# Kernel optimization log

Hardware: AMD Instinct MI355X
Metric: run time of the kernel (lower is better)

Reference implementation:

```python
import jax, jax.numpy as jnp
import numpy as np

# Module configuration (from init_kwargs)
N, C_IN, C_OUT, L, V, P = 4, 64, 64, 1024, 25, 3
KERNEL_SIZE, STRIDE = 9, 1
EPS = 1e-5


def _toeplitz(length):
    # Faithful to: sum_i pad(eye(L - stride*i), (i*stride, 0, 0, i*stride))
    # -> ones at [r, r + i*stride] for i in range(kernel_size // stride)
    t = jnp.zeros((length, length), dtype=jnp.float32)
    for i in range(KERNEL_SIZE // STRIDE):  # small fixed loop over taps
        t = t + jnp.eye(length, k=i * STRIDE, dtype=jnp.float32)
    return t


def setup_inputs() -> dict:
    key = jax.random.key(0)
    k0, k1, k2, k3 = jax.random.split(key, 4)
    x = jax.random.normal(k0, (N, C_IN, L, V), dtype=jnp.float32)
    A = jax.random.uniform(k1, (P, V, V), dtype=jnp.float32)
    edge_importance = jnp.ones((P, V, V), dtype=jnp.float32)
    conv_w = jax.random.normal(k2, (C_OUT * P, C_IN, 1, 1), dtype=jnp.float32) * 0.05
    conv_b = jax.random.normal(k3, (C_OUT * P,), dtype=jnp.float32) * 0.05
    gamma = jnp.ones((C_OUT,), dtype=jnp.float32)
    beta = jnp.zeros((C_OUT,), dtype=jnp.float32)
    return {"x": x, "A": A, "edge_importance": edge_importance,
            "conv_w": conv_w, "conv_b": conv_b, "gamma": gamma, "beta": beta}


def reference(x, A, edge_importance, conv_w, conv_b, gamma, beta):
    n, _, l, v = x.shape
    res = x  # residual: in_channels == out_channels and stride == 1 -> identity

    # 1x1 conv: (N, C_in, L, V) -> (N, P*C_out, L, V)
    w = conv_w[:, :, 0, 0]  # (P*C_out, C_in)
    y = jnp.einsum('nclv,kc->nklv', x, w) + conv_b[None, :, None, None]

    # split into P chunks of C_out along channels, stack, permute -> (N, L, P, C_out, V)
    y = y.reshape(n, P, C_OUT, l, v).transpose(0, 3, 1, 2, 4)

    # partition-wise graph adjacency matmul with edge-importance mask
    y = jnp.einsum('nlpcv,pvw->nlpcw', y, A * edge_importance)

    # Toeplitz temporal conv: (N, P, C, V, L) @ (L, L)
    y = y.transpose(0, 2, 3, 4, 1)
    y = jnp.matmul(y, _toeplitz(l))
    y = y.sum(axis=1)            # sum over partitions -> (N, C, V, L)
    y = y.transpose(0, 1, 3, 2)  # (N, C, L, V)

    # BatchNorm2d with batch statistics (track_running_stats=False) + ReLU
    mean = y.mean(axis=(0, 2, 3), keepdims=True)
    var = y.var(axis=(0, 2, 3), keepdims=True)  # biased, as torch uses for normalization
    y = (y - mean) * jax.lax.rsqrt(var + EPS)
    y = y * gamma[None, :, None, None] + beta[None, :, None, None]
    y = jax.nn.relu(y)

    # do = Sequential(ReLU, Dropout(0.0)) applied to (y + res)
    return jax.nn.relu(y + res)
```

## Files before the change

### kernel.cpp

```cpp
#include <hip/hip_runtime.h>
#include <hip/hip_cooperative_groups.h>

namespace cg = cooperative_groups;


typedef unsigned short ushort_t;
typedef __attribute__((ext_vector_type(8))) short short8;
typedef __attribute__((ext_vector_type(4))) float f32x4;
typedef __attribute__((ext_vector_type(4))) unsigned short us4;

#define N_  4
#define CI_ 64
#define CO_ 64
#define L_  1024
#define V_  25
#define P_  3
#define KS_ 9
#define NLV 102400.0f
#define NREP 32
#define TSTR 406

__device__ __forceinline__ float b2f(ushort_t u) {
  union { float f; unsigned int i; } c; c.i = ((unsigned int)u) << 16; return c.f;
}
__device__ __forceinline__ ushort_t f2b(float f) {
  union { float f; unsigned int i; } c; c.f = f;
  unsigned int u = c.i;
  u += 0x7fffu + ((u >> 16) & 1u);
  return (ushort_t)(u >> 16);
}
__device__ __forceinline__ unsigned int cvtpk(float lo, float hi) {
  unsigned int r;
  asm("v_cvt_pk_bf16_f32 %0, %1, %2" : "=v"(r) : "v"(lo), "v"(hi));
  return r;
}
__device__ __forceinline__ float lo2f(unsigned int u) {
  union { float f; unsigned int i; } c; c.i = u << 16; return c.f;
}
__device__ __forceinline__ float hi2f(unsigned int u) {
  union { float f; unsigned int i; } c; c.i = u & 0xffff0000u; return c.f;
}

__global__ __launch_bounds__(256) void kwin(
    const float* __restrict__ x, ushort_t* __restrict__ xs,
    const float* __restrict__ A, const float* __restrict__ E,
    const float* __restrict__ cb, const float* __restrict__ W,
    ushort_t* __restrict__ a2raw, float* __restrict__ biastab,
    ushort_t* __restrict__ wb, float* __restrict__ statsbuf)
{
  const int bx = blockIdx.x;
  const int n = blockIdx.y;
  const int tid = threadIdx.x;

  if (bx == 256) {
    if (n != 0) return;
    __shared__ float colA[P_ * 32];
    if (tid < P_ * 32) {
      int p = tid >> 5, w = tid & 31;
      float s = 0.f;
      if (w < V_)
        for (int v = 0; v < V_; ++v) {
          int idx = (p * V_ + v) * V_ + w;
          s += A[idx] * E[idx];
        }
      colA[tid] = s;
    }
    for (int e = tid; e < 32 * 96; e += 256) {
      int w = e / 96, k = e - w * 96;
      int p = k >> 5, v = k & 31;
      float val = 0.f;
      if (w < V_ && v < V_) {
        int idx = (p * V_ + v) * V_ + w;
        val = A[idx] * E[idx];
      }
      a2raw[e] = f2b(val);
    }
    for (int e = tid; e < 192 * 64; e += 256) wb[e] = f2b(W[e]);
    __syncthreads();
    for (int e = tid; e < 32 * 64; e += 256) {
      int w = e >> 6, c = e & 63;
      float s = 0.f;
      for (int p = 0; p < P_; ++p) s += cb[p * 64 + c] * colA[p * 32 + w];
      biastab[e] = s;
    }
    for (int e = tid; e < NREP * 128; e += 256) statsbuf[e] = 0.f;
    return;
  }

  const int chunk = bx >> 1, half = bx & 1;
  __shared__ __align__(16) ushort_t tile[32 * TSTR];
  const int l0 = chunk * 8;
  const long xn = (long)n * CI_ * L_ * V_ + (long)(half * 32) * (L_ * V_);
  for (int m = tid; m < 3200; m += 256) {
    int ci = m / 100;
    int j4 = (m - ci * 100) * 4;
    f32x4 d;
    if (chunk == 0 && j4 < 200) {
      d = (f32x4){0.f, 0.f, 0.f, 0.f};
    } else {
      d = *(const f32x4*)(x + xn + (long)ci * (L_ * V_) + (l0 - 8) * V_ + j4);
    }
    unsigned int p0 = (unsigned int)f2b(d[0]) | ((unsigned int)f2b(d[1]) << 16);
    unsigned int p1 = (unsigned int)f2b(d[2]) | ((unsigned int)f2b(d[3]) << 16);
    *(unsigned int*)(&tile[ci * TSTR + j4])     = p0;
    *(unsigned int*)(&tile[ci * TSTR + j4 + 2]) = p1;
  }
  __syncthreads();
  const long xsbase = ((long)n * L_ + l0) * 1600 + half * 32;
  for (int cp = tid; cp < 400; cp += 256) {
    const int v = cp >> 4, ci = (cp & 15) * 2;
    const ushort_t* c0 = &tile[ci * TSTR + v];
    const ushort_t* c1 = c0 + TSTR;
    float s0 = 0.f, s1 = 0.f;
#pragma unroll
    for (int li = 0; li < 9; ++li) { s0 += b2f(c0[li * 25]); s1 += b2f(c1[li * 25]); }
    *(unsigned int*)(xs + xsbase + v * 64 + ci) =
        (unsigned int)f2b(s0) | ((unsigned int)f2b(s1) << 16);
#pragma unroll
    for (int l_ = 1; l_ < 8; ++l_) {
      s0 += b2f(c0[(l_ + 8) * 25]) - b2f(c0[(l_ - 1) * 25]);
      s1 += b2f(c1[(l_ + 8) * 25]) - b2f(c1[(l_ - 1) * 25]);
      *(unsigned int*)(xs + xsbase + l_ * 1600 + v * 64 + ci) =
          (unsigned int)f2b(s0) | ((unsigned int)f2b(s1) << 16);
    }
  }
}

template<bool COOP>
__global__ __launch_bounds__(256, 4) void kmain(
    const float*    __restrict__ x,
    ushort_t*       __restrict__ xs,
    const float*    __restrict__ A, const float* __restrict__ E,
    const float*    __restrict__ cb, const float* __restrict__ W,
    ushort_t*       __restrict__ wb,
    ushort_t*       __restrict__ a2,
    float*          __restrict__ biastab,
    ushort_t*       __restrict__ zb,
    float*          __restrict__ statsbuf,
    const float*    __restrict__ gamma,
    const float*    __restrict__ beta,
    float*          __restrict__ out)
{
  const int lb = blockIdx.x;
  const int n  = blockIdx.y;
  const int tid = threadIdx.x, lane = tid & 63, wv = tid >> 6;
  const int m16 = lane & 15, quad = lane >> 4;

  __shared__ __align__(16) ushort_t T1[13312];
  __shared__ float colA[P_ * 32];

  if constexpr (COOP) {
    ushort_t* tile = T1;
    const int chunk = lb >> 1, half = lb & 1;
    const int l0 = chunk * 8;
    const long xn = (long)n * CI_ * L_ * V_ + (long)(half * 32) * (L_ * V_);
    for (int m = tid; m < 3200; m += 256) {
      int ci = m / 100;
      int j4 = (m - ci * 100) * 4;
      f32x4 d;
      if (chunk == 0 && j4 < 200) {
        d = (f32x4){0.f, 0.f, 0.f, 0.f};
      } else {
        d = *(const f32x4*)(x + xn + (long)ci * (L_ * V_) + (l0 - 8) * V_ + j4);
      }
      *(unsigned int*)(&tile[ci * TSTR + j4])     = cvtpk(d[0], d[1]);
      *(unsigned int*)(&tile[ci * TSTR + j4 + 2]) = cvtpk(d[2], d[3]);
    }
    if (n == 1) {
      if (lb == 0) {
        for (int e = tid; e < 32 * 96; e += 256) {
          int w = e / 96, k = e - w * 96;
          int p = k >> 5, v = k & 31;
          float val = 0.f;
          if (w < V_ && v < V_) {
            int idx = (p * V_ + v) * V_ + w;
            val = A[idx] * E[idx];
          }
          a2[e] = f2b(val);
        }
      } else if (lb == 1) {
        for (int e = tid; e < 6144; e += 256) wb[e] = f2b(W[e]);
      } else if (lb == 2) {
        for (int e = tid; e < 6144; e += 256) wb[6144 + e] = f2b(W[6144 + e]);
      } else if (lb == 3) {
        for (int e = tid; e < NREP * 128; e += 256) statsbuf[e] = 0.f;
      } else if (lb == 4) {
        if (tid < P_ * 32) {
          int p = tid >> 5, w = tid & 31;
          float s = 0.f;
          if (w < V_)
            for (int v = 0; v < V_; ++v) {
              int idx = (p * V_ + v) * V_ + w;
              s += A[idx] * E[idx];
            }
          colA[tid] = s;
        }
      }
    }
    __syncthreads();
    const long xsbase = ((long)n * L_ + l0) * 1600 + half * 32;
    for (int cp = tid; cp < 400; cp += 256) {
      const int v = cp >> 4, ci = (cp & 15) * 2;
      const ushort_t* c0 = &tile[ci * TSTR + v];
      const ushort_t* c1 = c0 + TSTR;
      float s0 = 0.f, s1 = 0.f;
#pragma unroll
      for (int li = 0; li < 9; ++li) { s0 += b2f(c0[li * 25]); s1 += b2f(c1[li * 25]); }
      *(unsigned int*)(xs + xsbase + v * 64 + ci) = cvtpk(s0, s1);
#pragma unroll
      for (int l_ = 1; l_ < 8; ++l_) {
        s0 += b2f(c0[(l_ + 8) * 25]) - b2f(c0[(l_ - 1) * 25]);
        s1 += b2f(c1[(l_ + 8) * 25]) - b2f(c1[(l_ - 1) * 25]);
        *(unsigned int*)(xs + xsbase + l_ * 1600 + v * 64 + ci) = cvtpk(s0, s1);
      }
    }
    if (n == 1 && lb == 4) {
      for (int e = tid; e < 32 * 64; e += 256) {
        int w = e >> 6, c = e & 63;
        float s = 0.f;
        for (int p = 0; p < P_; ++p) s += cb[p * 64 + c] * colA[p * 32 + w];
        biastab[e] = s;
      }
    }
    cg::this_grid().sync();
  }

  short8 af[3][2];
#pragma unroll
  for (int i = 0; i < 3; ++i) {
    const ushort_t* wrow = wb + ((wv * 3 + i) * 16 + m16) * 64 + quad * 8;
    af[i][0] = *(const short8*)(wrow);
    af[i][1] = *(const short8*)(wrow + 32);
  }

  short8 bfr2[2][3];
#pragma unroll
  for (int nt = 0; nt < 2; ++nt)
#pragma unroll
    for (int ks = 0; ks < 3; ++ks)
      bfr2[nt][ks] = *(const short8*)(a2 + (nt * 16 + m16) * 96 + ks * 32 + quad * 8);

  const int cbase = wv * 16 + quad * 4;
  f32x4 biasv[2];
#pragma unroll
  for (int nt = 0; nt < 2; ++nt)
    biasv[nt] = *(const f32x4*)(biastab + (nt * 16 + m16) * 64 + cbase);

  const ushort_t* xsb = xs + ((long)n * L_ + 4 * lb) * 1600;
  float s1[4] = {0.f, 0.f, 0.f, 0.f}, s2[4] = {0.f, 0.f, 0.f, 0.f};
  unsigned int zpk[2][2][2][2];

#pragma unroll
  for (int pair = 0; pair < 2; ++pair) {
    short8 bfr[4][2];
#pragma unroll
    for (int nt = 0; nt < 4; ++nt) {
      const int v = (nt & 1) * 16 + m16;
      const int l_ = pair * 2 + (nt >> 1);
#pragma unroll
      for (int ks = 0; ks < 2; ++ks) {
        short8 t = (short8){0, 0, 0, 0, 0, 0, 0, 0};
        if (v < V_)
          t = *(const short8*)(xsb + l_ * 1600 + v * 64 + ks * 32 + quad * 8);
        bfr[nt][ks] = t;
      }
    }

    f32x4 acc1[3][4];
#pragma unroll
    for (int i = 0; i < 3; ++i)
#pragma unroll
      for (int j = 0; j < 4; ++j) acc1[i][j] = (f32x4){0.f, 0.f, 0.f, 0.f};

#pragma unroll
    for (int i = 0; i < 3; ++i)
#pragma unroll
      for (int nt = 0; nt < 4; ++nt) {
        acc1[i][nt] = __builtin_amdgcn_mfma_f32_16x16x32_bf16(af[i][0], bfr[nt][0], acc1[i][nt], 0, 0, 0);
        acc1[i][nt] = __builtin_amdgcn_mfma_f32_16x16x32_bf16(af[i][1], bfr[nt][1], acc1[i][nt], 0, 0, 0);
      }

    __syncthreads();
#pragma unroll
    for (int i = 0; i < 3; ++i) {
      const int mt = wv * 3 + i;
#pragma unroll
      for (int nt = 0; nt < 4; ++nt) {
        const int l_ = nt >> 1;
        const int col = (nt & 1) * 16 + m16;
#pragma unroll
        for (int r = 0; r < 4; ++r) {
          int k = mt * 16 + quad * 4 + r;
          T1[l_ * 6656 + (k & 63) * 104 + (k >> 6) * 32 + col] = f2b(acc1[i][nt][r]);
        }
      }
    }
    __syncthreads();

    f32x4 acc2[2][2];
#pragma unroll
    for (int l_ = 0; l_ < 2; ++l_)
#pragma unroll
      for (int nt = 0; nt < 2; ++nt) acc2[l_][nt] = (f32x4){0.f, 0.f, 0.f, 0.f};

#pragma unroll
    for (int l_ = 0; l_ < 2; ++l_)
#pragma unroll
      for (int ks = 0; ks < 3; ++ks) {
        short8 afT = *(const short8*)(&T1[l_ * 6656 + (wv * 16 + m16) * 104 + ks * 32 + quad * 8]);
        acc2[l_][0] = __builtin_amdgcn_mfma_f32_16x16x32_bf16(afT, bfr2[0][ks], acc2[l_][0], 0, 0, 0);
        acc2[l_][1] = __builtin_amdgcn_mfma_f32_16x16x32_bf16(afT, bfr2[1][ks], acc2[l_][1], 0, 0, 0);
      }

#pragma unroll
    for (int l_ = 0; l_ < 2; ++l_) {
      const int l = 4 * lb + pair * 2 + l_;
      const float cnt = (float)(l + 1 < KS_ ? l + 1 : KS_);
#pragma unroll
      for (int nt = 0; nt < 2; ++nt) {
        const int w = nt * 16 + m16;
        if (w < V_) {
          const f32x4 bias = biasv[nt];
          const unsigned int u01 = cvtpk(acc2[l_][nt][0] + cnt * bias[0],
                                         acc2[l_][nt][1] + cnt * bias[1]);
          const unsigned int u23 = cvtpk(acc2[l_][nt][2] + cnt * bias[2],
                                         acc2[l_][nt][3] + cnt * bias[3]);
          const float z0 = lo2f(u01), z1 = hi2f(u01);
          const float z2 = lo2f(u23), z3 = hi2f(u23);
          s1[0] += z0; s2[0] += z0 * z0;
          s1[1] += z1; s2[1] += z1 * z1;
          s1[2] += z2; s2[2] += z2 * z2;
          s1[3] += z3; s2[3] += z3 * z3;
          if constexpr (COOP) {
            zpk[pair][l_][nt][0] = u01;
            zpk[pair][l_][nt][1] = u23;
          } else {
            ushort_t* zp = &zb[(((long)(n * L_ + l) * V_ + w) << 6) + cbase];
            *(unsigned int*)(zp)     = u01;
            *(unsigned int*)(zp + 2) = u23;
          }
        }
      }
    }
  }
#pragma unroll
  for (int off = 1; off < 16; off <<= 1) {
#pragma unroll
    for (int r = 0; r < 4; ++r) {
      s1[r] += __shfl_xor(s1[r], off, 64);
      s2[r] += __shfl_xor(s2[r], off, 64);
    }
  }
  if (m16 == 0) {
    float* sb = statsbuf + ((n * 256 + lb) & (NREP - 1)) * 128;
#pragma unroll
    for (int r = 0; r < 4; ++r) {
      atomicAdd(&sb[cbase + r], s1[r]);
      atomicAdd(&sb[64 + cbase + r], s2[r]);
    }
  }

  if constexpr (COOP) {
    __syncthreads();
    ushort_t* zl = T1;
#pragma unroll
    for (int pair = 0; pair < 2; ++pair)
#pragma unroll
      for (int l_ = 0; l_ < 2; ++l_)
#pragma unroll
        for (int nt = 0; nt < 2; ++nt) {
          const int w = nt * 16 + m16;
          if (w < V_) {
            const int rr = (pair * 2 + l_) * 25 + w;
            const int e = ((rr >> 2) & 31) << 1;
            *(unsigned int*)(&zl[rr * 68 + (cbase ^ e)])       = zpk[pair][l_][nt][0];
            *(unsigned int*)(&zl[rr * 68 + ((cbase + 2) ^ e)]) = zpk[pair][l_][nt][1];
          }
        }

    const long obase = (long)(n * 64) * (L_ * V_) + lb * 100;
    f32x4 xv[7];
#pragma unroll
    for (int i = 0; i < 7; ++i) {
      const int m = tid + i * 256;
      if (m < 1600) {
        const int c = m / 25, q = m - c * 25;
        xv[i] = *(const f32x4*)(x + obase + (long)c * (L_ * V_) + q * 4);
      }
    }

    cg::this_grid().sync();

    float* part = (float*)&T1[8192];
    float* scsh = (float*)&T1[8704];
    {
      const int slot = tid & 127, hf = tid >> 7;
      float a = 0.f;
      for (int k = hf; k < NREP; k += 2)
        a += __hip_atomic_load(&statsbuf[k * 128 + slot],
                               __ATOMIC_RELAXED, __HIP_MEMORY_SCOPE_AGENT);
      part[tid] = a;
    }
    __syncthreads();
    if (tid < 64) {
      const float inv = 1.0f / NLV;
      float s    = part[tid]      + part[128 + tid];
      float sq   = part[64 + tid] + part[192 + tid];
      float mean = s * inv;
      float var  = sq * inv - mean * mean;
      float rstd = rsqrtf(var + 1e-5f);
      float g = gamma[tid];
      scsh[tid]      = rstd * g;
      scsh[64 + tid] = beta[tid] - mean * rstd * g;
    }
    __syncthreads();

#pragma unroll
    for (int i = 0; i < 7; ++i) {
      const int m = tid + i * 256;
      if (m < 1600) {
        const int c = m / 25, q = m - c * 25, rr = q * 4;
        const int e = q << 1;
        const long xi = obase + (long)c * (L_ * V_) + rr;
        const float scc = scsh[c], shc = scsh[64 + c];
        f32x4 o;
#pragma unroll
        for (int j = 0; j < 4; ++j) {
          float z = b2f(zl[(rr + j) * 68 + (c ^ e)]);
          float y = fmaxf(z * scc + shc, 0.f);
          o[j] = fmaxf(y + xv[i][j], 0.f);
        }
        *(f32x4*)(out + xi) = o;
      }
    }
  }
}

__global__ __launch_bounds__(256) void kapply(
    const ushort_t* __restrict__ zb, const float* __restrict__ x,
    const float* __restrict__ statsbuf,
    const float* __restrict__ gamma, const float* __restrict__ beta,
    float* __restrict__ out)
{
  const int n = blockIdx.y, chunk = blockIdx.x;
  const int tid = threadIdx.x;
  __shared__ __align__(16) ushort_t zl[200 * 66];
  __shared__ f32x4 red[8][32];
  __shared__ float sc[64], sh[64];
  const long zbase = (long)((n * L_ + chunk * 8) * V_) * 64;
  for (int m = tid; m < 6400; m += 256) {
    const int row = m >> 5, c2 = (m & 31) * 2;
    const int cs = c2 ^ (((row >> 2) & 31) << 1);
    *(unsigned int*)(&zl[row * 66 + cs]) = ((const unsigned int*)(zb + zbase))[m];
  }
  {
    const int s4 = tid & 31, grp = tid >> 5;
    const f32x4* sb4 = (const f32x4*)statsbuf;
    f32x4 a = (f32x4){0.f, 0.f, 0.f, 0.f};
    for (int k = grp; k < NREP; k += 8) {
      f32x4 v = sb4[k * 32 + s4];
      a[0] += v[0]; a[1] += v[1]; a[2] += v[2]; a[3] += v[3];
    }
    red[grp][s4] = a;
  }
  __syncthreads();
  if (tid < 64) {
    const float inv = 1.0f / NLV;
    float s = 0.f, sq = 0.f;
#pragma unroll
    for (int g = 0; g < 8; ++g) {
      s  += red[g][tid >> 2][tid & 3];
      sq += red[g][16 + (tid >> 2)][tid & 3];
    }
    float mean = s * inv;
    float var  = sq * inv - mean * mean;
    float rstd = rsqrtf(var + 1e-5f);
    float g = gamma[tid];
    sc[tid] = rstd * g;
    sh[tid] = beta[tid] - mean * rstd * g;
  }
  __syncthreads();
  const long obase = ((long)(n * 64) * L_ + chunk * 8) * V_;
  for (int m = tid; m < 3200; m += 256) {
    int c = m / 50, q = m - c * 50, rr = q * 4;
    const int e = ((q & 31) << 1);
    long xi = obase + (long)c * (L_ * V_) + rr;
    f32x4 xv = *(const f32x4*)(x + xi);
    const float scc = sc[c], shc = sh[c];
    f32x4 o;
#pragma unroll
    for (int j = 0; j < 4; ++j) {
      float z = b2f(zl[(rr + j) * 66 + (c ^ e)]);
      float y = fmaxf(z * scc + shc, 0.f);
      o[j] = fmaxf(y + xv[j], 0.f);
    }
    *(f32x4*)(out + xi) = o;
  }
}

extern "C" void kernel_launch(void* const* d_in, const int* in_sizes, int n_in,
                              void* d_out, int out_size, void* d_ws, size_t ws_size,
                              hipStream_t stream)
{
  const float* x     = (const float*)d_in[0];
  const float* A     = (const float*)d_in[1];
  const float* E     = (const float*)d_in[2];
  const float* W     = (const float*)d_in[3];
  const float* cb    = (const float*)d_in[4];
  const float* gamma = (const float*)d_in[5];
  const float* beta  = (const float*)d_in[6];
  float* out = (float*)d_out;

  char* ws = (char*)d_ws;
  const size_t XS_OFF   = 0;
  const size_t ZB_OFF   = 13107200;
  const size_t WB_OFF   = 26214400;
  const size_t A2_OFF   = WB_OFF + 32768;
  const size_t BIAS_OFF = A2_OFF + 16384;
  const size_t STAT_OFF = BIAS_OFF + 16384;
  ushort_t* xs       = (ushort_t*)(ws + XS_OFF);
  ushort_t* zb       = (ushort_t*)(ws + ZB_OFF);
  ushort_t* wb       = (ushort_t*)(ws + WB_OFF);
  ushort_t* a2       = (ushort_t*)(ws + A2_OFF);
  float*    biastab  = (float*)(ws + BIAS_OFF);
  float*    statsbuf = (float*)(ws + STAT_OFF);

  auto kcoop = kmain<true>;
  int maxb = 0;
  hipError_t qe = hipOccupancyMaxActiveBlocksPerMultiprocessor(&maxb, kcoop, 256, 0);
  bool coop = (qe == hipSuccess) && (maxb >= 4);

  if (coop) {
    void* args[] = {(void*)&x, &xs, (void*)&A, (void*)&E, (void*)&cb, (void*)&W,
                    &wb, &a2, &biastab, &zb, &statsbuf,
                    (void*)&gamma, (void*)&beta, &out};
    hipError_t le = hipLaunchCooperativeKernel((const void*)kcoop,
                                               dim3(256, N_), dim3(256),
                                               args, 0, stream);
    if (le != hipSuccess) coop = false;
  }
  if (!coop) {
    kwin<<<dim3(257, N_), 256, 0, stream>>>(x, xs, A, E, cb, W, a2, biastab, wb,
                                            statsbuf);
    kmain<false><<<dim3(256, N_), 256, 0, stream>>>(
        x, xs, A, E, cb, W, wb, a2, biastab, zb, statsbuf, gamma, beta, out);
    kapply<<<dim3(128, N_), 256, 0, stream>>>(zb, x, statsbuf, gamma, beta, out);
  }
}
```

Before: 129.6 us.

## Drop first grid sync by having each block own full time window

Each cooperative block now handles 8 timesteps across all 64 input channels. It builds the windowed bf16 input sums it needs locally, so the first grid-wide sync can become a block barrier. The small parameter preprocessing (bf16 weights, adjacency, bias table, stats zeroing) moves to a separate tiny kprep launch before the cooperative kernel. The grid is halved to 128x4 blocks with larger LDS tiles and lower launch bounds, and the residual x is loaded after the remaining grid sync rather than prefetched. This trades one grid barrier for an extra kernel launch, fewer blocks in flight and more LDS per block.

```diff
diff --git a/kernel.cpp b/kernel.cpp
--- a/kernel.cpp
+++ b/kernel.cpp
@@ -18,7 +18,7 @@
 #define KS_ 9
 #define NLV 102400.0f
 #define NREP 32
-#define TSTR 406
+#define TSTR 402
 
 __device__ __forceinline__ float b2f(ushort_t u) {
   union { float f; unsigned int i; } c; c.i = ((unsigned int)u) << 16; return c.f;
@@ -39,6 +39,52 @@
 }
 __device__ __forceinline__ float hi2f(unsigned int u) {
   union { float f; unsigned int i; } c; c.i = u & 0xffff0000u; return c.f;
+}
+
+__global__ __launch_bounds__(256) void kprep(
+    const float* __restrict__ A, const float* __restrict__ E,
+    const float* __restrict__ W, const float* __restrict__ cb,
+    ushort_t* __restrict__ a2, float* __restrict__ biastab,
+    ushort_t* __restrict__ wb, float* __restrict__ statsbuf)
+{
+  const int b = blockIdx.x, tid = threadIdx.x;
+  if (b == 0) {
+    __shared__ float colA[P_ * 32];
+    if (tid < P_ * 32) {
+      int p = tid >> 5, w = tid & 31;
+      float s = 0.f;
+      if (w < V_)
+        for (int v = 0; v < V_; ++v) {
+          int idx = (p * V_ + v) * V_ + w;
+          s += A[idx] * E[idx];
+        }
+      colA[tid] = s;
+    }
+    __syncthreads();
+    for (int e = tid; e < 32 * 64; e += 256) {
+      int w = e >> 6, c = e & 63;
+      float s = 0.f;
+      for (int p = 0; p < P_; ++p) s += cb[p * 64 + c] * colA[p * 32 + w];
+      biastab[e] = s;
+    }
+  } else if (b == 1) {
+    for (int e = tid; e < 32 * 96; e += 256) {
+      int w = e / 96, k = e - w * 96;
+      int p = k >> 5, v = k & 31;
+      float val = 0.f;
+      if (w < V_ && v < V_) {
+        int idx = (p * V_ + v) * V_ + w;
+        val = A[idx] * E[idx];
+      }
+      a2[e] = f2b(val);
+    }
+  } else if (b < 4) {
+    const int base = (b - 2) * 6144;
+    for (int e = tid; e < 6144; e += 256) wb[base + e] = f2b(W[base + e]);
+  } else {
+    const int base = (b - 4) * 1024;
+    for (int e = tid; e < 1024; e += 256) statsbuf[base + e] = 0.f;
+  }
 }
 
 __global__ __launch_bounds__(256) void kwin(
@@ -88,7 +134,7 @@
   }
 
   const int chunk = bx >> 1, half = bx & 1;
-  __shared__ __align__(16) ushort_t tile[32 * TSTR];
+  __shared__ __align__(16) ushort_t tile[32 * 406];
   const int l0 = chunk * 8;
   const long xn = (long)n * CI_ * L_ * V_ + (long)(half * 32) * (L_ * V_);
   for (int m = tid; m < 3200; m += 256) {
@@ -100,41 +146,35 @@
     } else {
       d = *(const f32x4*)(x + xn + (long)ci * (L_ * V_) + (l0 - 8) * V_ + j4);
     }
-    unsigned int p0 = (unsigned int)f2b(d[0]) | ((unsigned int)f2b(d[1]) << 16);
-    unsigned int p1 = (unsigned int)f2b(d[2]) | ((unsigned int)f2b(d[3]) << 16);
-    *(unsigned int*)(&tile[ci * TSTR + j4])     = p0;
-    *(unsigned int*)(&tile[ci * TSTR + j4 + 2]) = p1;
+    *(unsigned int*)(&tile[ci * 406 + j4])     = cvtpk(d[0], d[1]);
+    *(unsigned int*)(&tile[ci * 406 + j4 + 2]) = cvtpk(d[2], d[3]);
   }
   __syncthreads();
   const long xsbase = ((long)n * L_ + l0) * 1600 + half * 32;
   for (int cp = tid; cp < 400; cp += 256) {
     const int v = cp >> 4, ci = (cp & 15) * 2;
-    const ushort_t* c0 = &tile[ci * TSTR + v];
-    const ushort_t* c1 = c0 + TSTR;
+    const ushort_t* c0 = &tile[ci * 406 + v];
+    const ushort_t* c1 = c0 + 406;
     float s0 = 0.f, s1 = 0.f;
 #pragma unroll
     for (int li = 0; li < 9; ++li) { s0 += b2f(c0[li * 25]); s1 += b2f(c1[li * 25]); }
-    *(unsigned int*)(xs + xsbase + v * 64 + ci) =
-        (unsigned int)f2b(s0) | ((unsigned int)f2b(s1) << 16);
+    *(unsigned int*)(xs + xsbase + v * 64 + ci) = cvtpk(s0, s1);
 #pragma unroll
     for (int l_ = 1; l_ < 8; ++l_) {
       s0 += b2f(c0[(l_ + 8) * 25]) - b2f(c0[(l_ - 1) * 25]);
       s1 += b2f(c1[(l_ + 8) * 25]) - b2f(c1[(l_ - 1) * 25]);
-      *(unsigned int*)(xs + xsbase + l_ * 1600 + v * 64 + ci) =
-          (unsigned int)f2b(s0) | ((unsigned int)f2b(s1) << 16);
+      *(unsigned int*)(xs + xsbase + l_ * 1600 + v * 64 + ci) = cvtpk(s0, s1);
     }
   }
 }
 
 template<bool COOP>
-__global__ __launch_bounds__(256, 4) void kmain(
+__global__ __launch_bounds__(256, 3) void kmain(
     const float*    __restrict__ x,
     ushort_t*       __restrict__ xs,
-    const float*    __restrict__ A, const float* __restrict__ E,
-    const float*    __restrict__ cb, const float* __restrict__ W,
-    ushort_t*       __restrict__ wb,
-    ushort_t*       __restrict__ a2,
-    float*          __restrict__ biastab,
+    const ushort_t* __restrict__ wb,
+    const ushort_t* __restrict__ a2,
+    const float*    __restrict__ biastab,
     ushort_t*       __restrict__ zb,
     float*          __restrict__ statsbuf,
     const float*    __restrict__ gamma,
@@ -146,19 +186,18 @@
   const int tid = threadIdx.x, lane = tid & 63, wv = tid >> 6;
   const int m16 = lane & 15, quad = lane >> 4;
 
-  __shared__ __align__(16) ushort_t T1[13312];
-  __shared__ float colA[P_ * 32];
+  __shared__ __align__(16) ushort_t tile[64 * TSTR];
+  ushort_t* T1 = tile;
+
+  const int l0 = lb * 8;
 
   if constexpr (COOP) {
-    ushort_t* tile = T1;
-    const int chunk = lb >> 1, half = lb & 1;
-    const int l0 = chunk * 8;
-    const long xn = (long)n * CI_ * L_ * V_ + (long)(half * 32) * (L_ * V_);
-    for (int m = tid; m < 3200; m += 256) {
+    const long xn = (long)n * CI_ * L_ * V_;
+    for (int m = tid; m < 6400; m += 256) {
       int ci = m / 100;
       int j4 = (m - ci * 100) * 4;
       f32x4 d;
-      if (chunk == 0 && j4 < 200) {
+      if (lb == 0 && j4 < 200) {
         d = (f32x4){0.f, 0.f, 0.f, 0.f};
       } else {
         d = *(const f32x4*)(x + xn + (long)ci * (L_ * V_) + (l0 - 8) * V_ + j4);
@@ -166,41 +205,10 @@
       *(unsigned int*)(&tile[ci * TSTR + j4])     = cvtpk(d[0], d[1]);
       *(unsigned int*)(&tile[ci * TSTR + j4 + 2]) = cvtpk(d[2], d[3]);
     }
-    if (n == 1) {
-      if (lb == 0) {
-        for (int e = tid; e < 32 * 96; e += 256) {
-          int w = e / 96, k = e - w * 96;
-          int p = k >> 5, v = k & 31;
-          float val = 0.f;
-          if (w < V_ && v < V_) {
-            int idx = (p * V_ + v) * V_ + w;
-            val = A[idx] * E[idx];
-          }
-          a2[e] = f2b(val);
-        }
-      } else if (lb == 1) {
-        for (int e = tid; e < 6144; e += 256) wb[e] = f2b(W[e]);
-      } else if (lb == 2) {
-        for (int e = tid; e < 6144; e += 256) wb[6144 + e] = f2b(W[6144 + e]);
-      } else if (lb == 3) {
-        for (int e = tid; e < NREP * 128; e += 256) statsbuf[e] = 0.f;
-      } else if (lb == 4) {
-        if (tid < P_ * 32) {
-          int p = tid >> 5, w = tid & 31;
-          float s = 0.f;
-          if (w < V_)
-            for (int v = 0; v < V_; ++v) {
-              int idx = (p * V_ + v) * V_ + w;
-              s += A[idx] * E[idx];
-            }
-          colA[tid] = s;
-        }
-      }
-    }
-    __syncthreads();
-    const long xsbase = ((long)n * L_ + l0) * 1600 + half * 32;
-    for (int cp = tid; cp < 400; cp += 256) {
-      const int v = cp >> 4, ci = (cp & 15) * 2;
+    __syncthreads();
+    const long xsbase = ((long)n * L_ + l0) * 1600;
+    for (int cp = tid; cp < 800; cp += 256) {
+      const int v = cp >> 5, ci = (cp & 31) * 2;
       const ushort_t* c0 = &tile[ci * TSTR + v];
       const ushort_t* c1 = c0 + TSTR;
       float s0 = 0.f, s1 = 0.f;
@@ -214,15 +222,7 @@
         *(unsigned int*)(xs + xsbase + l_ * 1600 + v * 64 + ci) = cvtpk(s0, s1);
       }
     }
-    if (n == 1 && lb == 4) {
-      for (int e = tid; e < 32 * 64; e += 256) {
-        int w = e >> 6, c = e & 63;
-        float s = 0.f;
-        for (int p = 0; p < P_; ++p) s += cb[p * 64 + c] * colA[p * 32 + w];
-        biastab[e] = s;
-      }
-    }
-    cg::this_grid().sync();
+    __syncthreads();
   }
 
   short8 af[3][2];
@@ -232,7 +232,6 @@
     af[i][0] = *(const short8*)(wrow);
     af[i][1] = *(const short8*)(wrow + 32);
   }
-
   short8 bfr2[2][3];
 #pragma unroll
   for (int nt = 0; nt < 2; ++nt)
@@ -246,12 +245,12 @@
   for (int nt = 0; nt < 2; ++nt)
     biasv[nt] = *(const f32x4*)(biastab + (nt * 16 + m16) * 64 + cbase);
 
-  const ushort_t* xsb = xs + ((long)n * L_ + 4 * lb) * 1600;
+  const ushort_t* xsb = xs + ((long)n * L_ + l0) * 1600;
   float s1[4] = {0.f, 0.f, 0.f, 0.f}, s2[4] = {0.f, 0.f, 0.f, 0.f};
-  unsigned int zpk[2][2][2][2];
-
-#pragma unroll
-  for (int pair = 0; pair < 2; ++pair) {
+  unsigned int zpk[4][2][2][2];
+
+#pragma unroll
+  for (int pair = 0; pair < 4; ++pair) {
     short8 bfr[4][2];
 #pragma unroll
     for (int nt = 0; nt < 4; ++nt) {
@@ -280,7 +279,7 @@
         acc1[i][nt] = __builtin_amdgcn_mfma_f32_16x16x32_bf16(af[i][1], bfr[nt][1], acc1[i][nt], 0, 0, 0);
       }
 
-    __syncthreads();
+    if (pair) __syncthreads();
 #pragma unroll
     for (int i = 0; i < 3; ++i) {
       const int mt = wv * 3 + i;
@@ -314,7 +313,7 @@
 
 #pragma unroll
     for (int l_ = 0; l_ < 2; ++l_) {
-      const int l = 4 * lb + pair * 2 + l_;
+      const int l = l0 + pair * 2 + l_;
       const float cnt = (float)(l + 1 < KS_ ? l + 1 : KS_);
 #pragma unroll
       for (int nt = 0; nt < 2; ++nt) {
@@ -352,7 +351,7 @@
     }
   }
   if (m16 == 0) {
-    float* sb = statsbuf + ((n * 256 + lb) & (NREP - 1)) * 128;
+    float* sb = statsbuf + ((n * 128 + lb) & (NREP - 1)) * 128;
 #pragma unroll
     for (int r = 0; r < 4; ++r) {
       atomicAdd(&sb[cbase + r], s1[r]);
@@ -362,9 +361,9 @@
 
   if constexpr (COOP) {
     __syncthreads();
-    ushort_t* zl = T1;
-#pragma unroll
-    for (int pair = 0; pair < 2; ++pair)
+    ushort_t* zl = tile;
+#pragma unroll
+    for (int pair = 0; pair < 4; ++pair)
 #pragma unroll
       for (int l_ = 0; l_ < 2; ++l_)
 #pragma unroll
@@ -378,21 +377,10 @@
           }
         }
 
-    const long obase = (long)(n * 64) * (L_ * V_) + lb * 100;
-    f32x4 xv[7];
-#pragma unroll
-    for (int i = 0; i < 7; ++i) {
-      const int m = tid + i * 256;
-      if (m < 1600) {
-        const int c = m / 25, q = m - c * 25;
-        xv[i] = *(const f32x4*)(x + obase + (long)c * (L_ * V_) + q * 4);
-      }
-    }
-
     cg::this_grid().sync();
 
-    float* part = (float*)&T1[8192];
-    float* scsh = (float*)&T1[8704];
+    float* part = (float*)&tile[13952];
+    float* scsh = (float*)&tile[14464];
     {
       const int slot = tid & 127, hf = tid >> 7;
       float a = 0.f;
@@ -415,23 +403,21 @@
     }
     __syncthreads();
 
-#pragma unroll
-    for (int i = 0; i < 7; ++i) {
-      const int m = tid + i * 256;
-      if (m < 1600) {
-        const int c = m / 25, q = m - c * 25, rr = q * 4;
-        const int e = q << 1;
-        const long xi = obase + (long)c * (L_ * V_) + rr;
-        const float scc = scsh[c], shc = scsh[64 + c];
-        f32x4 o;
-#pragma unroll
-        for (int j = 0; j < 4; ++j) {
-          float z = b2f(zl[(rr + j) * 68 + (c ^ e)]);
-          float y = fmaxf(z * scc + shc, 0.f);
-          o[j] = fmaxf(y + xv[i][j], 0.f);
-        }
-        *(f32x4*)(out + xi) = o;
-      }
+    const long obase = (long)(n * 64) * (L_ * V_) + lb * 200;
+    for (int m = tid; m < 3200; m += 256) {
+      const int c = m / 50, q = m - c * 50, rr = q * 4;
+      const int e = (q & 31) << 1;
+      const long xi = obase + (long)c * (L_ * V_) + rr;
+      const f32x4 xv = *(const f32x4*)(x + xi);
+      const float scc = scsh[c], shc = scsh[64 + c];
+      f32x4 o;
+#pragma unroll
+      for (int j = 0; j < 4; ++j) {
+        float z = b2f(zl[(rr + j) * 68 + (c ^ e)]);
+        float y = fmaxf(z * scc + shc, 0.f);
+        o[j] = fmaxf(y + xv[j], 0.f);
+      }
+      *(f32x4*)(out + xi) = o;
     }
   }
 }
@@ -528,22 +514,22 @@
   auto kcoop = kmain<true>;
   int maxb = 0;
   hipError_t qe = hipOccupancyMaxActiveBlocksPerMultiprocessor(&maxb, kcoop, 256, 0);
-  bool coop = (qe == hipSuccess) && (maxb >= 4);
+  bool coop = (qe == hipSuccess) && (maxb >= 2);
 
   if (coop) {
-    void* args[] = {(void*)&x, &xs, (void*)&A, (void*)&E, (void*)&cb, (void*)&W,
-                    &wb, &a2, &biastab, &zb, &statsbuf,
+    kprep<<<dim3(8), 256, 0, stream>>>(A, E, W, cb, a2, biastab, wb, statsbuf);
+    void* args[] = {(void*)&x, &xs, &wb, &a2, &biastab, &zb, &statsbuf,
                     (void*)&gamma, (void*)&beta, &out};
     hipError_t le = hipLaunchCooperativeKernel((const void*)kcoop,
-                                               dim3(256, N_), dim3(256),
+                                               dim3(128, N_), dim3(256),
                                                args, 0, stream);
     if (le != hipSuccess) coop = false;
   }
   if (!coop) {
     kwin<<<dim3(257, N_), 256, 0, stream>>>(x, xs, A, E, cb, W, a2, biastab, wb,
                                             statsbuf);
-    kmain<false><<<dim3(256, N_), 256, 0, stream>>>(
-        x, xs, A, E, cb, W, wb, a2, biastab, zb, statsbuf, gamma, beta, out);
+    kmain<false><<<dim3(128, N_), 256, 0, stream>>>(
+        x, xs, wb, a2, biastab, zb, statsbuf, gamma, beta, out);
     kapply<<<dim3(128, N_), 256, 0, stream>>>(zb, x, statsbuf, gamma, beta, out);
   }
 }
```

Measured after the change: 127.3 us. No clear change (-1.8%).
